# Performance work log

Measured on AMD Instinct MI355X. Metric: run time of the kernel, lower is better.

Reference implementation:

```python
import jax, jax.numpy as jnp
import numpy as np
from jax import lax

EPS = 1e-8


def setup_inputs() -> dict:
    key = jax.random.key(0)
    ks = jax.random.split(key, 8)
    B, Cin, Cout, Wd, H, Wi, K = 16, 512, 512, 512, 64, 64, 3
    x = jax.random.normal(ks[0], (B, Cin, H, Wi), dtype=jnp.float32)
    w = jax.random.normal(ks[1], (B, Wd), dtype=jnp.float32)
    noise = jax.random.normal(ks[2], (B, 1, H, Wi), dtype=jnp.float32)
    # EqualizedLinear params (weight stored as N(0,1), runtime scale 1/sqrt(w_dim)); bias init 1.0
    w_style = jax.random.normal(ks[3], (Cin, Wd), dtype=jnp.float32)
    b_style = jnp.ones((Cin,), dtype=jnp.float32)
    # ConvModLayer equalized weight, stored N(0,1), runtime scale 1/sqrt(Cin*K*K)
    w_conv = jax.random.normal(ks[4], (Cout, Cin, K, K), dtype=jnp.float32)
    scale_noise = 0.1 * jax.random.normal(ks[5], (1,), dtype=jnp.float32)
    bias = 0.1 * jax.random.normal(ks[6], (Cout,), dtype=jnp.float32)
    return {"x": x, "w": w, "noise": noise, "w_style": w_style, "b_style": b_style,
            "w_conv": w_conv, "scale_noise": scale_noise, "bias": bias}


def reference(x, w, noise, w_style, b_style, w_conv, scale_noise, bias):
    B, Cin, H, W = x.shape
    Cout, _, K, _ = w_conv.shape
    # to_style: equalized linear, A = w @ (w_style / sqrt(w_dim)).T + b_style
    c_lin = 1.0 / jnp.sqrt(jnp.float32(w_style.shape[1]))
    A = w @ (w_style * c_lin).T + b_style  # [B, Cin]
    # modulated conv (equalized conv weight scale)
    c_conv = 1.0 / jnp.sqrt(jnp.float32(Cin * K * K))
    wts = (w_conv * c_conv)[None] * A[:, None, :, None, None]  # [B, Cout, Cin, K, K]
    demod = lax.rsqrt(jnp.sum(wts * wts, axis=(2, 3, 4), keepdims=True) + EPS)
    wts = wts * demod
    # grouped-conv batch trick: groups = B
    xg = x.reshape(1, B * Cin, H, W)
    wg = wts.reshape(B * Cout, Cin, K, K)
    out = lax.conv_general_dilated(xg, wg, (1, 1), 'SAME',
                                   feature_group_count=B,
                                   dimension_numbers=('NCHW', 'OIHW', 'NCHW'))
    out = out.reshape(B, Cout, H, W)
    out = out + scale_noise[None, :, None, None] * noise
    out = out + bias[None, :, None, None]
    return jnp.where(out >= 0, out, 0.2 * out)  # LeakyReLU(0.2)
```

## Files before the change

kernel.cpp:

```cpp
#include <hip/hip_runtime.h>
#include <stdint.h>


typedef __attribute__((ext_vector_type(8))) short s16x8;
typedef __attribute__((ext_vector_type(4))) float f32x4;

constexpr int CIN = 512, COUT = 512, WD = 512, HW = 4096;
constexpr float C_LIN  = 0.04419417382415922f;
constexpr float C_CONV = 0.014731391274719739f;
constexpr float CC2    = 1.0f / 4608.0f;

constexpr int WSEG = 2304;

constexpr size_t WS_A = 0, WS_S = 32768;
constexpr size_t WS_WP = 1310720, WS_XT = 6291456;

__device__ __forceinline__ unsigned short f2bf(float f) {
  union { float f; unsigned int u; } v; v.f = f;
  unsigned int u = v.u + 0x7FFFu + ((v.u >> 16) & 1u);
  return (unsigned short)(u >> 16);
}

__device__ __forceinline__ void gload16(const void* g, void* l) {
  __builtin_amdgcn_global_load_lds((const __attribute__((address_space(1))) void*)g,
                                   (__attribute__((address_space(3))) void*)l, 16, 0, 0);
}

__global__ void k_sw(const float* __restrict__ wc, uint4* __restrict__ wp,
                     float* __restrict__ S) {
  __shared__ float wt[64][289];
  const int ct = blockIdx.x, ch = blockIdx.y, tid = threadIdx.x;
  const int co0 = ct * 64, ci0 = ch * 32;
  for (int i = tid; i < 64 * 288; i += 256) {
    int co = i / 288, r = i - co * 288;
    wt[co][r] = wc[(size_t)(co0 + co) * 4608 + (size_t)ci0 * 9 + r];
  }
  __syncthreads();
  uint4* seg = wp + (size_t)(ct * 16 + ch) * WSEG;
  for (int c = tid; c < 2304; c += 256) {
    int t = c >> 8, rem = c & 255, s = rem >> 6, co = rem & 63;
    union { unsigned short u[8]; uint4 v; } pk;
#pragma unroll
    for (int j = 0; j < 8; ++j) pk.u[j] = f2bf(wt[co][(s*8 + j) * 9 + t] * C_CONV);
    seg[(t * 4 + s) * 64 + co] = pk.v;
  }
  for (int i = tid; i < 2048; i += 256) {
    int co = i >> 5, ci = i & 31;
    float s_ = 0.f;
#pragma unroll
    for (int t = 0; t < 9; ++t) { float v = wt[co][ci * 9 + t]; s_ += v * v; }
    S[(size_t)(co0 + co) * CIN + ci0 + ci] = s_;
  }
}

__global__ __launch_bounds__(256) void k_xta(
    const float* __restrict__ x, const float* __restrict__ w,
    const float* __restrict__ wsty, const float* __restrict__ bs,
    float* __restrict__ A, uint4* __restrict__ xt) {
  __shared__ float wl[WD];
  __shared__ float red[256];
  __shared__ float As[32];
  const int p = blockIdx.x, b = blockIdx.y, tid = threadIdx.x;
  const int ch = p >> 2, rowgrp = p & 3, ci0 = ch * 32;
  for (int i = tid; i < WD; i += 256) wl[i] = w[b * WD + i];
  __syncthreads();
  const int ci_l = tid >> 3, part = tid & 7;
  {
    const float4* row = (const float4*)(wsty + (size_t)(ci0 + ci_l) * WD + part * 64);
    float acc = 0.f;
#pragma unroll
    for (int k = 0; k < 16; ++k) {
      float4 v = row[k];
      acc += v.x * wl[part*64 + 4*k] + v.y * wl[part*64 + 4*k+1]
           + v.z * wl[part*64 + 4*k+2] + v.w * wl[part*64 + 4*k+3];
    }
    red[tid] = acc;
  }
  __syncthreads();
  if (part == 0) {
    float s = 0.f;
#pragma unroll
    for (int q = 0; q < 8; ++q) s += red[ci_l * 8 + q];
    float a = s * C_LIN + bs[ci0 + ci_l];
    As[ci_l] = a;
    if (rowgrp == 0) A[b * CIN + ci0 + ci_l] = a;
  }
  __syncthreads();
  const int lane = tid & 63, wave = tid >> 6;
  const float* xb = x + ((size_t)(b * CIN + ci0) << 12) + lane;
  uint4* dstb = xt + (size_t)((b << 4) + ch) * 16896;
#pragma unroll
  for (int i = 0; i < 4; ++i) {
    const int rw = rowgrp * 16 + wave * 4 + i;
    const float* xr = xb + (rw << 6);
    uint4* dst = dstb + (size_t)(rw * 4) * 66;
#pragma unroll
    for (int s = 0; s < 4; ++s) {
      union { unsigned short u[8]; uint4 v; } pk;
#pragma unroll
      for (int j = 0; j < 8; ++j)
        pk.u[j] = f2bf(xr[(size_t)(s * 8 + j) << 12] * As[s * 8 + j]);
      dst[s * 66 + 1 + lane] = pk.v;
      if (lane < 2) dst[s * 66 + lane * 65] = (uint4){0, 0, 0, 0};
    }
  }
}

__global__ __launch_bounds__(512, 2) void k_conv(
    const uint4* __restrict__ xt, const uint4* __restrict__ wp,
    const float* __restrict__ S, const float* __restrict__ A,
    const float* __restrict__ noise, const float* __restrict__ sn_,
    const float* __restrict__ bias, float* __restrict__ out) {

  __shared__ __align__(16) uint4 x_lds[2][2640];
  __shared__ __align__(16) uint4 w_lds[2][WSEG];
  __shared__ float red[512];
  __shared__ float dm_l[64], bi_l[64];

  const int sp = blockIdx.x, ct = blockIdx.y, b = blockIdx.z;
  const int r0 = sp * 8, co0 = ct * 64;
  const int tid = threadIdx.x, lane = tid & 63, wave = tid >> 6;
  const int l15 = lane & 15, l4 = lane >> 4;

  const int lo = (r0 - 1 > 0) ? r0 - 1 : 0;
  const int hi = (r0 + 8 < 63) ? r0 + 8 : 63;
  const int cells = (hi - lo + 1) * 264;
  const int dst0 = (lo - (r0 - 1)) * 264;

  auto stage = [&](int buf, int ch) {
    const uint4* xsrc = xt + ((size_t)(b * 16 + ch) * 64 + lo) * 264;
    for (int i = wave; i * 64 < cells; i += 8)
      if (i * 64 + lane < cells)
        gload16(xsrc + i * 64 + lane, &x_lds[buf][dst0 + i * 64]);
    const uint4* wsrc = wp + (size_t)(ct * 16 + ch) * WSEG;
    for (int i = wave; i < 36; i += 8)
      gload16(wsrc + i * 64 + lane, &w_lds[buf][i * 64]);
  };

  stage(0, 0);

  if (sp == 0) for (int i = tid; i < 264; i += 512) {
    x_lds[0][i] = (uint4){0,0,0,0}; x_lds[1][i] = (uint4){0,0,0,0};
  }
  if (sp == 7) for (int i = tid; i < 264; i += 512) {
    x_lds[0][2376+i] = (uint4){0,0,0,0}; x_lds[1][2376+i] = (uint4){0,0,0,0};
  }

  {
    const int co = tid >> 3, part = tid & 7;
    const float4* srow = (const float4*)(S + (size_t)(co0 + co) * CIN + part * 64);
    const float4* arow = (const float4*)(A + (size_t)b * CIN + part * 64);
    float acc = 0.f;
#pragma unroll
    for (int k = 0; k < 16; ++k) {
      float4 sv = srow[k], av = arow[k];
      acc += sv.x*av.x*av.x + sv.y*av.y*av.y + sv.z*av.z*av.z + sv.w*av.w*av.w;
    }
    red[tid] = acc;
  }
  __syncthreads();
  if (tid < 64) {
    float s_ = 0.f;
#pragma unroll
    for (int q = 0; q < 8; ++q) s_ += red[tid * 8 + q];
    dm_l[tid] = rsqrtf(CC2 * s_ + 1e-8f);
    bi_l[tid] = bias[co0 + tid];
  }

  f32x4 acc[4][4];
#pragma unroll
  for (int m = 0; m < 4; ++m)
#pragma unroll
    for (int f = 0; f < 4; ++f) acc[m][f] = (f32x4){0.f, 0.f, 0.f, 0.f};

  __syncthreads();

  for (int ch = 0; ch < 16; ++ch) {
    const int buf = ch & 1;
    if (ch < 15) stage(buf ^ 1, ch + 1);

#pragma unroll
    for (int t = 0; t < 9; ++t) {
      const int dh = t / 3, dw = t - dh * 3;
      s16x8 afr[4], bfr[4];
#pragma unroll
      for (int m = 0; m < 4; ++m)
        afr[m] = *(const s16x8*)&w_lds[buf][(t * 4 + l4) * 64 + m * 16 + l15];
#pragma unroll
      for (int f = 0; f < 4; ++f)
        bfr[f] = *(const s16x8*)&x_lds[buf][((wave + dh) * 4 + l4) * 66 + f * 16 + l15 + dw];
      __builtin_amdgcn_s_setprio(1);
#pragma unroll
      for (int m = 0; m < 4; ++m)
#pragma unroll
        for (int f = 0; f < 4; ++f)
          acc[m][f] = __builtin_amdgcn_mfma_f32_16x16x32_bf16(afr[m], bfr[f], acc[m][f], 0, 0, 0);
      __builtin_amdgcn_s_setprio(0);
    }
    __syncthreads();
  }

  const float sn = sn_[0];
  const int row = r0 + wave;
  float nz[4];
#pragma unroll
  for (int f = 0; f < 4; ++f) nz[f] = sn * noise[b * HW + row * 64 + f * 16 + l15];
#pragma unroll
  for (int m = 0; m < 4; ++m) {
#pragma unroll
    for (int reg = 0; reg < 4; ++reg) {
      const int co_l = m * 16 + l4 * 4 + reg;
      const float d = dm_l[co_l], bv = bi_l[co_l];
      float* op = out + ((size_t)(b * COUT + co0 + co_l)) * HW + row * 64;
#pragma unroll
      for (int f = 0; f < 4; ++f) {
        float v = d * acc[m][f][reg] + nz[f] + bv;
        op[f * 16 + l15] = (v >= 0.f) ? v : 0.2f * v;
      }
    }
  }
}

extern "C" void kernel_launch(void* const* d_in, const int* in_sizes, int n_in,
                              void* d_out, int out_size, void* d_ws, size_t ws_size,
                              hipStream_t stream) {
  (void)in_sizes; (void)n_in; (void)out_size; (void)ws_size;
  const float* x           = (const float*)d_in[0];
  const float* w           = (const float*)d_in[1];
  const float* noise       = (const float*)d_in[2];
  const float* w_style     = (const float*)d_in[3];
  const float* b_style     = (const float*)d_in[4];
  const float* w_conv      = (const float*)d_in[5];
  const float* scale_noise = (const float*)d_in[6];
  const float* bias        = (const float*)d_in[7];
  float* out = (float*)d_out;

  char* ws = (char*)d_ws;
  float* A     = (float*)(ws + WS_A);
  float* S     = (float*)(ws + WS_S);
  uint4* wpack = (uint4*)(ws + WS_WP);
  uint4* xt    = (uint4*)(ws + WS_XT);

  k_sw<<<dim3(8, 16), 256, 0, stream>>>(w_conv, wpack, S);
  k_xta<<<dim3(64, 16), 256, 0, stream>>>(x, w, w_style, b_style, A, xt);
  k_conv<<<dim3(8, 8, 16), 512, 0, stream>>>(xt, wpack, S, A, noise, scale_noise, bias, out);
}
```

Measured before the change: 546.8 us.

## Single-buffer LDS with DPP-shifted x fragments to raise conv occupancy

The conv kernel drops LDS double buffering and keeps one x tile and one weight tile, raising launch bounds from 2 to 4 blocks per CU. Instead of three LDS reads per kernel row (one per horizontal tap), it reads the x fragments once per row and builds the dw=1,2 shifts with DPP row shifts, taking the wrap-around element from a small separate edge array. The x staging layout changes to a 64-wide main segment plus an edge segment, and the denominator and bias scratch reuse the reduction buffer. The cost is that loads are no longer overlapped with MFMA inside a block, and there are two barriers per channel chunk, relying on the higher occupancy to hide latency.

After: 544.9 us. About the same (-0.3%).

```diff
diff --git a/kernel.cpp b/kernel.cpp
--- a/kernel.cpp
+++ b/kernel.cpp
@@ -11,6 +11,7 @@
 constexpr float CC2    = 1.0f / 4608.0f;
 
 constexpr int WSEG = 2304;
+constexpr int XSEG = 16640;
 
 constexpr size_t WS_A = 0, WS_S = 32768;
 constexpr size_t WS_WP = 1310720, WS_XT = 6291456;
@@ -24,6 +25,22 @@
 __device__ __forceinline__ void gload16(const void* g, void* l) {
   __builtin_amdgcn_global_load_lds((const __attribute__((address_space(1))) void*)g,
                                    (__attribute__((address_space(3))) void*)l, 16, 0, 0);
+}
+
+union I4H8 { int4 i; s16x8 h; uint4 u; };
+
+template <int CA, int CB>
+__device__ __forceinline__ int4 dmix(int4 a, int4 b) {
+  int4 r;
+  r.x = __builtin_amdgcn_mov_dpp(a.x, CA, 0xF, 0xF, true) |
+        __builtin_amdgcn_mov_dpp(b.x, CB, 0xF, 0xF, true);
+  r.y = __builtin_amdgcn_mov_dpp(a.y, CA, 0xF, 0xF, true) |
+        __builtin_amdgcn_mov_dpp(b.y, CB, 0xF, 0xF, true);
+  r.z = __builtin_amdgcn_mov_dpp(a.z, CA, 0xF, 0xF, true) |
+        __builtin_amdgcn_mov_dpp(b.z, CB, 0xF, 0xF, true);
+  r.w = __builtin_amdgcn_mov_dpp(a.w, CA, 0xF, 0xF, true) |
+        __builtin_amdgcn_mov_dpp(b.w, CB, 0xF, 0xF, true);
+  return r;
 }
 
 __global__ void k_sw(const float* __restrict__ wc, uint4* __restrict__ wp,
@@ -87,63 +104,75 @@
   }
   __syncthreads();
   const int lane = tid & 63, wave = tid >> 6;
-  const float* xb = x + ((size_t)(b * CIN + ci0) << 12) + lane;
-  uint4* dstb = xt + (size_t)((b << 4) + ch) * 16896;
+  const int px = (lane == 0) ? 63 : lane - 1;
+  const float* xb = x + ((size_t)(b * CIN + ci0) << 12) + px;
+  uint4* seg = xt + (size_t)((b << 4) + ch) * XSEG;
 #pragma unroll
   for (int i = 0; i < 4; ++i) {
-    const int rw = rowgrp * 16 + wave * 4 + i;
-    const float* xr = xb + (rw << 6);
-    uint4* dst = dstb + (size_t)(rw * 4) * 66;
+    const int row = rowgrp * 16 + wave * 4 + i;
+    const float* xr = xb + (row << 6);
 #pragma unroll
     for (int s = 0; s < 4; ++s) {
       union { unsigned short u[8]; uint4 v; } pk;
 #pragma unroll
       for (int j = 0; j < 8; ++j)
         pk.u[j] = f2bf(xr[(size_t)(s * 8 + j) << 12] * As[s * 8 + j]);
-      dst[s * 66 + 1 + lane] = pk.v;
-      if (lane < 2) dst[s * 66 + lane * 65] = (uint4){0, 0, 0, 0};
-    }
-  }
-}
-
-__global__ __launch_bounds__(512, 2) void k_conv(
+      if (lane == 0) {
+        seg[16384 + row * 4 + s] = pk.v;
+        seg[(row * 4 + s) * 64] = (uint4){0, 0, 0, 0};
+      } else {
+        seg[(row * 4 + s) * 64 + lane] = pk.v;
+      }
+    }
+  }
+}
+
+__global__ __launch_bounds__(512, 4) void k_conv(
     const uint4* __restrict__ xt, const uint4* __restrict__ wp,
     const float* __restrict__ S, const float* __restrict__ A,
     const float* __restrict__ noise, const float* __restrict__ sn_,
     const float* __restrict__ bias, float* __restrict__ out) {
 
-  __shared__ __align__(16) uint4 x_lds[2][2640];
-  __shared__ __align__(16) uint4 w_lds[2][WSEG];
+  __shared__ __align__(16) uint4 xm_lds[2560];
+  __shared__ __align__(16) uint4 xe_lds[40];
+  __shared__ __align__(16) uint4 w_lds[WSEG];
   __shared__ float red[512];
-  __shared__ float dm_l[64], bi_l[64];
 
   const int sp = blockIdx.x, ct = blockIdx.y, b = blockIdx.z;
   const int r0 = sp * 8, co0 = ct * 64;
   const int tid = threadIdx.x, lane = tid & 63, wave = tid >> 6;
   const int l15 = lane & 15, l4 = lane >> 4;
+  const bool l15z = (l15 == 0);
 
   const int lo = (r0 - 1 > 0) ? r0 - 1 : 0;
   const int hi = (r0 + 8 < 63) ? r0 + 8 : 63;
-  const int cells = (hi - lo + 1) * 264;
-  const int dst0 = (lo - (r0 - 1)) * 264;
-
-  auto stage = [&](int buf, int ch) {
-    const uint4* xsrc = xt + ((size_t)(b * 16 + ch) * 64 + lo) * 264;
-    for (int i = wave; i * 64 < cells; i += 8)
-      if (i * 64 + lane < cells)
-        gload16(xsrc + i * 64 + lane, &x_lds[buf][dst0 + i * 64]);
+  const int nrows = hi - lo + 1;
+  const int dst0 = (lo - (r0 - 1)) * 256;
+  const int edst0 = (lo - (r0 - 1)) * 4;
+
+  auto stage = [&](int ch) {
+    const uint4* seg = xt + (size_t)(b * 16 + ch) * XSEG;
+    const uint4* xsrc = seg + (size_t)lo * 256;
+    const int nI = nrows * 4;
+    for (int i = wave; i < nI; i += 8)
+      gload16(xsrc + i * 64 + lane, &xm_lds[dst0 + i * 64]);
+    const uint4* esrc = seg + 16384 + lo * 4;
+    if (wave == 0 && lane < nrows * 4)
+      gload16(esrc + lane, &xe_lds[edst0 + lane]);
     const uint4* wsrc = wp + (size_t)(ct * 16 + ch) * WSEG;
     for (int i = wave; i < 36; i += 8)
-      gload16(wsrc + i * 64 + lane, &w_lds[buf][i * 64]);
+      gload16(wsrc + i * 64 + lane, &w_lds[i * 64]);
   };
 
-  stage(0, 0);
-
-  if (sp == 0) for (int i = tid; i < 264; i += 512) {
-    x_lds[0][i] = (uint4){0,0,0,0}; x_lds[1][i] = (uint4){0,0,0,0};
-  }
-  if (sp == 7) for (int i = tid; i < 264; i += 512) {
-    x_lds[0][2376+i] = (uint4){0,0,0,0}; x_lds[1][2376+i] = (uint4){0,0,0,0};
+  stage(0);
+
+  if (sp == 0) {
+    for (int i = tid; i < 256; i += 512) xm_lds[i] = (uint4){0, 0, 0, 0};
+    if (tid < 4) xe_lds[tid] = (uint4){0, 0, 0, 0};
+  }
+  if (sp == 7) {
+    for (int i = tid; i < 256; i += 512) xm_lds[2304 + i] = (uint4){0, 0, 0, 0};
+    if (tid < 4) xe_lds[36 + tid] = (uint4){0, 0, 0, 0};
   }
 
   {
@@ -159,12 +188,15 @@
     red[tid] = acc;
   }
   __syncthreads();
+  float dmv = 0.f;
   if (tid < 64) {
-    float s_ = 0.f;
-#pragma unroll
-    for (int q = 0; q < 8; ++q) s_ += red[tid * 8 + q];
-    dm_l[tid] = rsqrtf(CC2 * s_ + 1e-8f);
-    bi_l[tid] = bias[co0 + tid];
+#pragma unroll
+    for (int q = 0; q < 8; ++q) dmv += red[tid * 8 + q];
+  }
+  __syncthreads();
+  if (tid < 64) {
+    red[tid] = rsqrtf(CC2 * dmv + 1e-8f);
+    red[64 + tid] = bias[co0 + tid];
   }
 
   f32x4 acc[4][4];
@@ -172,31 +204,49 @@
   for (int m = 0; m < 4; ++m)
 #pragma unroll
     for (int f = 0; f < 4; ++f) acc[m][f] = (f32x4){0.f, 0.f, 0.f, 0.f};
-
   __syncthreads();
 
   for (int ch = 0; ch < 16; ++ch) {
-    const int buf = ch & 1;
-    if (ch < 15) stage(buf ^ 1, ch + 1);
-
-#pragma unroll
-    for (int t = 0; t < 9; ++t) {
-      const int dh = t / 3, dw = t - dh * 3;
-      s16x8 afr[4], bfr[4];
-#pragma unroll
-      for (int m = 0; m < 4; ++m)
-        afr[m] = *(const s16x8*)&w_lds[buf][(t * 4 + l4) * 64 + m * 16 + l15];
-#pragma unroll
-      for (int f = 0; f < 4; ++f)
-        bfr[f] = *(const s16x8*)&x_lds[buf][((wave + dh) * 4 + l4) * 66 + f * 16 + l15 + dw];
-      __builtin_amdgcn_s_setprio(1);
-#pragma unroll
-      for (int m = 0; m < 4; ++m)
-#pragma unroll
-        for (int f = 0; f < 4; ++f)
-          acc[m][f] = __builtin_amdgcn_mfma_f32_16x16x32_bf16(afr[m], bfr[f], acc[m][f], 0, 0, 0);
-      __builtin_amdgcn_s_setprio(0);
-    }
+#pragma unroll
+    for (int dh = 0; dh < 3; ++dh) {
+      const int rb = (wave + dh) * 4 + l4;
+      I4H8 d0[4], eF;
+#pragma unroll
+      for (int f = 0; f < 4; ++f) d0[f].u = xm_lds[rb * 64 + f * 16 + l15];
+      {
+        I4H8 e; e.u = xe_lds[rb];
+        eF.i.x = l15z ? e.i.x : 0;
+        eF.i.y = l15z ? e.i.y : 0;
+        eF.i.z = l15z ? e.i.z : 0;
+        eF.i.w = l15z ? e.i.w : 0;
+      }
+#pragma unroll
+      for (int dw = 0; dw < 3; ++dw) {
+        I4H8 bf[4];
+        if (dw == 0) {
+#pragma unroll
+          for (int f = 0; f < 4; ++f) bf[f] = d0[f];
+        } else if (dw == 1) {
+#pragma unroll
+          for (int f = 0; f < 4; ++f)
+            bf[f].i = dmix<0x101, 0x11F>(d0[f].i, (f < 3) ? d0[f + 1].i : eF.i);
+        } else {
+#pragma unroll
+          for (int f = 0; f < 4; ++f)
+            bf[f].i = dmix<0x102, 0x11E>(d0[f].i, (f < 3) ? d0[f + 1].i : eF.i);
+        }
+        const int t = dh * 3 + dw;
+#pragma unroll
+        for (int m = 0; m < 4; ++m) {
+          s16x8 a = *(const s16x8*)&w_lds[(t * 4 + l4) * 64 + m * 16 + l15];
+#pragma unroll
+          for (int f = 0; f < 4; ++f)
+            acc[m][f] = __builtin_amdgcn_mfma_f32_16x16x32_bf16(a, bf[f].h, acc[m][f], 0, 0, 0);
+        }
+      }
+    }
+    __syncthreads();
+    if (ch < 15) stage(ch + 1);
     __syncthreads();
   }
 
@@ -210,7 +260,7 @@
 #pragma unroll
     for (int reg = 0; reg < 4; ++reg) {
       const int co_l = m * 16 + l4 * 4 + reg;
-      const float d = dm_l[co_l], bv = bi_l[co_l];
+      const float d = red[co_l], bv = red[64 + co_l];
       float* op = out + ((size_t)(b * COUT + co0 + co_l)) * HW + row * 64;
 #pragma unroll
       for (int f = 0; f < 4; ++f) {
```
